# Performance work log

Measured on AMD Instinct MI355X. Metric: run time of the kernel, lower is better.

## Reference

```python
import jax, jax.numpy as jnp
import numpy as np

B, C, F = 4, 3, 5
HO, WO = 256, 256
HI, WI = HO + F - 1, WO + F - 1


def setup_inputs() -> dict:
    key = jax.random.key(0)
    k = jax.random.split(key, 6)
    return {
        "tensorInput": jax.random.normal(k[0], (B, C, HI, WI), dtype=jnp.float32),
        "tensorVertical": jax.random.uniform(k[1], (B, F, HO, WO), dtype=jnp.float32),
        "tensorHorizontal": jax.random.uniform(k[2], (B, F, HO, WO), dtype=jnp.float32),
        "tensorOffsetX": jax.random.normal(k[3], (B, F * F, HO, WO), dtype=jnp.float32),
        "tensorOffsetY": jax.random.normal(k[4], (B, F * F, HO, WO), dtype=jnp.float32),
        "tensorMask": jax.random.uniform(k[5], (B, F * F, HO, WO), dtype=jnp.float32),
    }


def _dsepconv(inp, vertical, horizontal, offset_x, offset_y, mask):
    b, c, hin, win = inp.shape
    f = vertical.shape[1]
    ho, wo = vertical.shape[2], vertical.shape[3]
    half = (f - 1) / 2.0

    fy = jnp.arange(f, dtype=inp.dtype).reshape(f, 1, 1, 1)
    fx = jnp.arange(f, dtype=inp.dtype).reshape(1, f, 1, 1)
    hg = jnp.arange(ho, dtype=inp.dtype).reshape(1, 1, ho, 1)
    wg = jnp.arange(wo, dtype=inp.dtype).reshape(1, 1, 1, wo)

    off_y = offset_y.reshape(b, f, f, ho, wo)  # note: code uses offset_y for delta_x
    off_x = offset_x.reshape(b, f, f, ho, wo)  # and offset_x for delta_y

    # sample positions per tap, [B,F,F,Ho,Wo]
    px = jnp.clip(off_y + wg + fx - half + 1.0, 0.0, win - 1)
    py = jnp.clip(off_x + hg + fy - half + 1.0, 0.0, hin - 1)

    left_f = jnp.floor(px)
    top_f = jnp.floor(py)
    wx = 1.0 - (px - left_f)  # bilinear weights
    wy = 1.0 - (py - top_f)

    l = left_f.astype(jnp.int32)
    t = top_f.astype(jnp.int32)
    r = jnp.minimum(l + 1, win - 1)
    btm = jnp.minimum(t + 1, hin - 1)

    def gather(img, yi, xi):
        return img[:, yi, xi]

    g = jax.vmap(gather)
    v_tl = g(inp, t, l)
    v_tr = g(inp, t, r)
    v_bl = g(inp, btm, l)
    v_br = g(inp, btm, r)

    wx_ = wx[:, None]  # add channel axis -> [B,1,F,F,Ho,Wo]
    wy_ = wy[:, None]
    val = (v_tl * wx_ * wy_ + v_tr * (1 - wx_) * wy_
           + v_bl * wx_ * (1 - wy_) + v_br * (1 - wx_) * (1 - wy_))

    # separable filter x mask per tap: [B,F,F,Ho,Wo]
    w_tap = vertical[:, :, None] * horizontal[:, None, :] * mask.reshape(b, f, f, ho, wo)
    # accumulate over the F*F taps
    return jnp.sum(val * w_tap[:, None], axis=(2, 3))  # [B,C,Ho,Wo]


def reference(tensorInput, tensorVertical, tensorHorizontal, tensorOffsetX, tensorOffsetY, tensorMask):
    return _dsepconv(tensorInput, tensorVertical, tensorHorizontal,
                     tensorOffsetX, tensorOffsetY, tensorMask)
```

## Files before the change

### kernel.cpp

```cpp
#include <hip/hip_runtime.h>
#include <hip/hip_fp16.h>

constexpr int B  = 4;
constexpr int C  = 3;
constexpr int F  = 5;
constexpr int HO = 256;
constexpr int WO = 256;
constexpr int HI = HO + F - 1;
constexpr int WI = WO + F - 1;
constexpr int P  = HO * WO;
constexpr int FF = F * F;
constexpr int PI = HI * WI;

constexpr int TROWS = 21;
constexpr int TCOLS = 80;
constexpr int TSTRIDE = 81;
constexpr int TN = TROWS * TCOLS;
constexpr int AMAX = (TROWS - 2) * TSTRIDE + (TCOLS - 2);

__device__ __forceinline__ uint2 pack3(float a, float b, float c) {
    __half2 ab = __floats2half2_rn(a, b);
    __half2 cz = __floats2half2_rn(c, 0.0f);
    uint2 r;
    r.x = *reinterpret_cast<const unsigned int*>(&ab);
    r.y = *reinterpret_cast<const unsigned int*>(&cz);
    return r;
}

__device__ __forceinline__ void fmacc(uint2 v, float w,
                                      float& a0, float& a1, float& a2) {
    __half2 ab = *reinterpret_cast<const __half2*>(&v.x);
    __half2 cz = *reinterpret_cast<const __half2*>(&v.y);
    a0 += __half2float(__low2half(ab))  * w;
    a1 += __half2float(__high2half(ab)) * w;
    a2 += __half2float(__low2half(cz))  * w;
}

__global__ __launch_bounds__(512, 8) void dsepconv_kernel(
    const float* __restrict__ inp,
    const float* __restrict__ vert,
    const float* __restrict__ horz,
    const float* __restrict__ offX,
    const float* __restrict__ offY,
    const float* __restrict__ mask,
    float* __restrict__ out)
{
    __shared__ uint2 tileq[TROWS * TSTRIDE];
    __shared__ float red[4][3][64];

    const int tid  = threadIdx.x;
    const int lane = tid & 63;
    const int wave = tid >> 6;
    const int wrow = wave >> 1;
    const int half = wave & 1;

    const int bx   = blockIdx.x;
    const int x0   = (bx & 3) * 64;
    const int y0   = ((bx >> 2) & 63) * 4;
    const int b    = bx >> 8;

    const float* in0 = inp + (size_t)b * C * PI;
    const float* in1 = in0 + PI;
    const float* in2 = in1 + PI;

    const int ry0 = y0 - 7;
    const int cx0 = x0 - 7;
#pragma unroll 1
    for (int e = tid; e < TN; e += 512) {
        int trow = e / TCOLS;
        int tcol = e - trow * TCOLS;
        int gy = min(max(ry0 + trow, 0), HI - 1);
        int gx = min(max(cx0 + tcol, 0), WI - 1);
        int g = gy * WI + gx;
        tileq[trow * TSTRIDE + tcol] = pack3(in0[g], in1[g], in2[g]);
    }
    __syncthreads();

    const int x   = x0 + lane;
    const int y   = y0 + wrow;
    const int pix = y * WO + x;

    const float* offXb = offX + (size_t)b * FF * P + pix;
    const float* offYb = offY + (size_t)b * FF * P + pix;
    const float* maskb = mask + (size_t)b * FF * P + pix;
    const float* vb    = vert + (size_t)b * F * P + pix;
    const float* hb    = horz + (size_t)b * F * P + pix;

    float acc0 = 0.f, acc1 = 0.f, acc2 = 0.f;

    const int k0 = half ? 12 : 0;
    const int k1 = half ? 25 : 12;

#pragma unroll 1
    for (int k = k0; k < k1; ++k) {
        const int i = k / F;
        const int j = k - i * F;

        float oy = offYb[k * P];
        float ox = offXb[k * P];
        float m  = maskb[k * P];
        float h  = hb[j * P];
        float v  = vb[i * P];

        float px = fminf(fmaxf(oy + (float)(x + j - 1), 0.0f), (float)(WI - 1));
        float py = fminf(fmaxf(ox + (float)(y + i - 1), 0.0f), (float)(HI - 1));

        float lf = floorf(px);
        float tf = floorf(py);
        int l = (int)lf;
        int t = (int)tf;
        float wx = 1.0f - (px - lf);
        float wy = 1.0f - (py - tf);

        float w   = v * h * m;
        float wyw = wy * w;
        float wbw = w - wyw;
        float wtl = wx * wyw;
        float wtr = wyw - wtl;
        float wbl = wx * wbw;
        float wbr = wbw - wbl;

        int lt = t - ry0;
        int ll = l - cx0;
        bool ok = ((unsigned)lt <= TROWS - 2) & ((unsigned)ll <= TCOLS - 2);

        int a = min(max(lt * TSTRIDE + ll, 0), AMAX);

        uint2 g_tl = tileq[a];
        uint2 g_tr = tileq[a + 1];
        uint2 g_bl = tileq[a + TSTRIDE];
        uint2 g_br = tileq[a + TSTRIDE + 1];

        if (__any(!ok)) {
            if (!ok) {
                int r  = min(l + 1, WI - 1);
                int bt = min(t + 1, HI - 1);
                int o_tl = t * WI + l,  o_tr = t * WI + r;
                int o_bl = bt * WI + l, o_br = bt * WI + r;
                g_tl = pack3(in0[o_tl], in1[o_tl], in2[o_tl]);
                g_tr = pack3(in0[o_tr], in1[o_tr], in2[o_tr]);
                g_bl = pack3(in0[o_bl], in1[o_bl], in2[o_bl]);
                g_br = pack3(in0[o_br], in1[o_br], in2[o_br]);
            }
        }

        fmacc(g_tl, wtl, acc0, acc1, acc2);
        fmacc(g_tr, wtr, acc0, acc1, acc2);
        fmacc(g_bl, wbl, acc0, acc1, acc2);
        fmacc(g_br, wbr, acc0, acc1, acc2);
    }

    if (half) {
        red[wrow][0][lane] = acc0;
        red[wrow][1][lane] = acc1;
        red[wrow][2][lane] = acc2;
    }
    __syncthreads();

    if (!half) {
        float* ob = out + (size_t)b * C * P + pix;
        ob[0]     = acc0 + red[wrow][0][lane];
        ob[P]     = acc1 + red[wrow][1][lane];
        ob[2 * P] = acc2 + red[wrow][2][lane];
    }
}

extern "C" void kernel_launch(void* const* d_in, const int* in_sizes, int n_in,
                              void* d_out, int out_size, void* d_ws, size_t ws_size,
                              hipStream_t stream) {
    const float* inp  = (const float*)d_in[0];
    const float* vert = (const float*)d_in[1];
    const float* horz = (const float*)d_in[2];
    const float* offX = (const float*)d_in[3];
    const float* offY = (const float*)d_in[4];
    const float* mask = (const float*)d_in[5];
    float* out = (float*)d_out;

    dim3 block(512);
    dim3 grid(B * (HO / 4) * (WO / 64));
    dsepconv_kernel<<<grid, block, 0, stream>>>(inp, vert, horz, offX, offY, mask, out);
}
```

Baseline: 26.54 us.

## Process two pixels per thread with float2 loads and prefetch next tap

Measured after the change: 24.75 us. 1.07x faster.

```diff
diff --git a/kernel.cpp b/kernel.cpp
--- a/kernel.cpp
+++ b/kernel.cpp
@@ -12,11 +12,15 @@
 constexpr int FF = F * F;
 constexpr int PI = HI * WI;
 
-constexpr int TROWS = 21;
-constexpr int TCOLS = 80;
-constexpr int TSTRIDE = 81;
+constexpr int TROWS = 19;
+constexpr int TCOLS = 145;
+constexpr int TSTRIDE = 149;
 constexpr int TN = TROWS * TCOLS;
 constexpr int AMAX = (TROWS - 2) * TSTRIDE + (TCOLS - 2);
+
+__device__ __forceinline__ float2 ld2(const float* p) {
+    return *reinterpret_cast<const float2*>(p);
+}
 
 __device__ __forceinline__ uint2 pack3(float a, float b, float c) {
     __half2 ab = __floats2half2_rn(a, b);
@@ -36,7 +40,7 @@
     a2 += __half2float(__low2half(cz))  * w;
 }
 
-__global__ __launch_bounds__(512, 8) void dsepconv_kernel(
+__global__ __launch_bounds__(256, 4) void dsepconv_kernel(
     const float* __restrict__ inp,
     const float* __restrict__ vert,
     const float* __restrict__ horz,
@@ -46,7 +50,7 @@
     float* __restrict__ out)
 {
     __shared__ uint2 tileq[TROWS * TSTRIDE];
-    __shared__ float red[4][3][64];
+    __shared__ float red[2][3][128];
 
     const int tid  = threadIdx.x;
     const int lane = tid & 63;
@@ -55,18 +59,41 @@
     const int half = wave & 1;
 
     const int bx   = blockIdx.x;
-    const int x0   = (bx & 3) * 64;
-    const int y0   = ((bx >> 2) & 63) * 4;
+    const int x0   = (bx & 1) * 128;
+    const int y0   = ((bx >> 1) & 127) * 2;
     const int b    = bx >> 8;
 
     const float* in0 = inp + (size_t)b * C * PI;
     const float* in1 = in0 + PI;
     const float* in2 = in1 + PI;
 
+    const int x   = x0 + 2 * lane;
+    const int y   = y0 + wrow;
+    const int pix = y * WO + x;
+
+    const float* offXb = offX + (size_t)b * FF * P + pix;
+    const float* offYb = offY + (size_t)b * FF * P + pix;
+    const float* maskb = mask + (size_t)b * FF * P + pix;
+    const float* vb    = vert + (size_t)b * F * P + pix;
+    const float* hb    = horz + (size_t)b * F * P + pix;
+
+    const int k0 = half ? 12 : 0;
+    const int k1 = half ? 25 : 12;
+
+    float2 oy, ox, m, h, v;
+    {
+        const int i = k0 / F, j = k0 - (k0 / F) * F;
+        oy = ld2(offYb + (size_t)k0 * P);
+        ox = ld2(offXb + (size_t)k0 * P);
+        m  = ld2(maskb + (size_t)k0 * P);
+        h  = ld2(hb + (size_t)j * P);
+        v  = ld2(vb + (size_t)i * P);
+    }
+
     const int ry0 = y0 - 7;
     const int cx0 = x0 - 7;
 #pragma unroll 1
-    for (int e = tid; e < TN; e += 512) {
+    for (int e = tid; e < TN; e += 256) {
         int trow = e / TCOLS;
         int tcol = e - trow * TCOLS;
         int gy = min(max(ry0 + trow, 0), HI - 1);
@@ -76,92 +103,118 @@
     }
     __syncthreads();
 
-    const int x   = x0 + lane;
-    const int y   = y0 + wrow;
-    const int pix = y * WO + x;
-
-    const float* offXb = offX + (size_t)b * FF * P + pix;
-    const float* offYb = offY + (size_t)b * FF * P + pix;
-    const float* maskb = mask + (size_t)b * FF * P + pix;
-    const float* vb    = vert + (size_t)b * F * P + pix;
-    const float* hb    = horz + (size_t)b * F * P + pix;
-
-    float acc0 = 0.f, acc1 = 0.f, acc2 = 0.f;
-
-    const int k0 = half ? 12 : 0;
-    const int k1 = half ? 25 : 12;
+    float acc0a = 0.f, acc1a = 0.f, acc2a = 0.f;
+    float acc0b = 0.f, acc1b = 0.f, acc2b = 0.f;
 
 #pragma unroll 1
     for (int k = k0; k < k1; ++k) {
         const int i = k / F;
         const int j = k - i * F;
 
-        float oy = offYb[k * P];
-        float ox = offXb[k * P];
-        float m  = maskb[k * P];
-        float h  = hb[j * P];
-        float v  = vb[i * P];
-
-        float px = fminf(fmaxf(oy + (float)(x + j - 1), 0.0f), (float)(WI - 1));
-        float py = fminf(fmaxf(ox + (float)(y + i - 1), 0.0f), (float)(HI - 1));
-
-        float lf = floorf(px);
-        float tf = floorf(py);
-        int l = (int)lf;
-        int t = (int)tf;
-        float wx = 1.0f - (px - lf);
-        float wy = 1.0f - (py - tf);
-
-        float w   = v * h * m;
-        float wyw = wy * w;
-        float wbw = w - wyw;
-        float wtl = wx * wyw;
-        float wtr = wyw - wtl;
-        float wbl = wx * wbw;
-        float wbr = wbw - wbl;
-
-        int lt = t - ry0;
-        int ll = l - cx0;
-        bool ok = ((unsigned)lt <= TROWS - 2) & ((unsigned)ll <= TCOLS - 2);
-
-        int a = min(max(lt * TSTRIDE + ll, 0), AMAX);
-
-        uint2 g_tl = tileq[a];
-        uint2 g_tr = tileq[a + 1];
-        uint2 g_bl = tileq[a + TSTRIDE];
-        uint2 g_br = tileq[a + TSTRIDE + 1];
-
-        if (__any(!ok)) {
-            if (!ok) {
-                int r  = min(l + 1, WI - 1);
-                int bt = min(t + 1, HI - 1);
-                int o_tl = t * WI + l,  o_tr = t * WI + r;
-                int o_bl = bt * WI + l, o_br = bt * WI + r;
-                g_tl = pack3(in0[o_tl], in1[o_tl], in2[o_tl]);
-                g_tr = pack3(in0[o_tr], in1[o_tr], in2[o_tr]);
-                g_bl = pack3(in0[o_bl], in1[o_bl], in2[o_bl]);
-                g_br = pack3(in0[o_br], in1[o_br], in2[o_br]);
+        const int kn  = (k + 1 < k1) ? k + 1 : k;
+        const int in_ = kn / F;
+        const int jn  = kn - in_ * F;
+        float2 oy_n = ld2(offYb + (size_t)kn * P);
+        float2 ox_n = ld2(offXb + (size_t)kn * P);
+        float2 m_n  = ld2(maskb + (size_t)kn * P);
+        float2 h_n  = ld2(hb + (size_t)jn * P);
+        float2 v_n  = ld2(vb + (size_t)in_ * P);
+
+        float pya = fminf(fmaxf(ox.x + (float)(y + i - 1), 0.0f), (float)(HI - 1));
+        float pyb = fminf(fmaxf(ox.y + (float)(y + i - 1), 0.0f), (float)(HI - 1));
+        float pxa = fminf(fmaxf(oy.x + (float)(x + j - 1), 0.0f), (float)(WI - 1));
+        float pxb = fminf(fmaxf(oy.y + (float)(x + j), 0.0f), (float)(WI - 1));
+
+        float lfa = floorf(pxa), tfa = floorf(pya);
+        float lfb = floorf(pxb), tfb = floorf(pyb);
+        int la = (int)lfa, ta = (int)tfa;
+        int lb = (int)lfb, tb = (int)tfb;
+        float wxa = 1.0f - (pxa - lfa), wya = 1.0f - (pya - tfa);
+        float wxb = 1.0f - (pxb - lfb), wyb = 1.0f - (pyb - tfb);
+
+        int lta = ta - ry0, lla = la - cx0;
+        int ltb = tb - ry0, llb = lb - cx0;
+        bool oka = ((unsigned)lta <= TROWS - 2) & ((unsigned)lla <= TCOLS - 2);
+        bool okb = ((unsigned)ltb <= TROWS - 2) & ((unsigned)llb <= TCOLS - 2);
+
+        int aa = min(max(lta * TSTRIDE + lla, 0), AMAX);
+        int ab = min(max(ltb * TSTRIDE + llb, 0), AMAX);
+
+        uint2 ga0 = tileq[aa];
+        uint2 ga1 = tileq[aa + 1];
+        uint2 ga2 = tileq[aa + TSTRIDE];
+        uint2 ga3 = tileq[aa + TSTRIDE + 1];
+        uint2 gb0 = tileq[ab];
+        uint2 gb1 = tileq[ab + 1];
+        uint2 gb2 = tileq[ab + TSTRIDE];
+        uint2 gb3 = tileq[ab + TSTRIDE + 1];
+
+        if (__any(!(oka & okb))) {
+            if (!oka) {
+                int r  = min(la + 1, WI - 1);
+                int bt = min(ta + 1, HI - 1);
+                int o0 = ta * WI + la, o1 = ta * WI + r;
+                int o2 = bt * WI + la, o3 = bt * WI + r;
+                ga0 = pack3(in0[o0], in1[o0], in2[o0]);
+                ga1 = pack3(in0[o1], in1[o1], in2[o1]);
+                ga2 = pack3(in0[o2], in1[o2], in2[o2]);
+                ga3 = pack3(in0[o3], in1[o3], in2[o3]);
+            }
+            if (!okb) {
+                int r  = min(lb + 1, WI - 1);
+                int bt = min(tb + 1, HI - 1);
+                int o0 = tb * WI + lb, o1 = tb * WI + r;
+                int o2 = bt * WI + lb, o3 = bt * WI + r;
+                gb0 = pack3(in0[o0], in1[o0], in2[o0]);
+                gb1 = pack3(in0[o1], in1[o1], in2[o1]);
+                gb2 = pack3(in0[o2], in1[o2], in2[o2]);
+                gb3 = pack3(in0[o3], in1[o3], in2[o3]);
             }
         }
 
-        fmacc(g_tl, wtl, acc0, acc1, acc2);
-        fmacc(g_tr, wtr, acc0, acc1, acc2);
-        fmacc(g_bl, wbl, acc0, acc1, acc2);
-        fmacc(g_br, wbr, acc0, acc1, acc2);
+        float wA   = v.x * h.x * m.x;
+        float wywA = wya * wA;
+        float wbwA = wA - wywA;
+        float wtlA = wxa * wywA;
+        float wtrA = wywA - wtlA;
+        float wblA = wxa * wbwA;
+        float wbrA = wbwA - wblA;
+
+        float wB   = v.y * h.y * m.y;
+        float wywB = wyb * wB;
+        float wbwB = wB - wywB;
+        float wtlB = wxb * wywB;
+        float wtrB = wywB - wtlB;
+        float wblB = wxb * wbwB;
+        float wbrB = wbwB - wblB;
+
+        fmacc(ga0, wtlA, acc0a, acc1a, acc2a);
+        fmacc(ga1, wtrA, acc0a, acc1a, acc2a);
+        fmacc(ga2, wblA, acc0a, acc1a, acc2a);
+        fmacc(ga3, wbrA, acc0a, acc1a, acc2a);
+        fmacc(gb0, wtlB, acc0b, acc1b, acc2b);
+        fmacc(gb1, wtrB, acc0b, acc1b, acc2b);
+        fmacc(gb2, wblB, acc0b, acc1b, acc2b);
+        fmacc(gb3, wbrB, acc0b, acc1b, acc2b);
+
+        oy = oy_n; ox = ox_n; m = m_n; h = h_n; v = v_n;
     }
 
     if (half) {
-        red[wrow][0][lane] = acc0;
-        red[wrow][1][lane] = acc1;
-        red[wrow][2][lane] = acc2;
+        *reinterpret_cast<float2*>(&red[wrow][0][2 * lane]) = make_float2(acc0a, acc0b);
+        *reinterpret_cast<float2*>(&red[wrow][1][2 * lane]) = make_float2(acc1a, acc1b);
+        *reinterpret_cast<float2*>(&red[wrow][2][2 * lane]) = make_float2(acc2a, acc2b);
     }
     __syncthreads();
 
     if (!half) {
         float* ob = out + (size_t)b * C * P + pix;
-        ob[0]     = acc0 + red[wrow][0][lane];
-        ob[P]     = acc1 + red[wrow][1][lane];
-        ob[2 * P] = acc2 + red[wrow][2][lane];
+        float2 r0 = *reinterpret_cast<const float2*>(&red[wrow][0][2 * lane]);
+        float2 r1 = *reinterpret_cast<const float2*>(&red[wrow][1][2 * lane]);
+        float2 r2 = *reinterpret_cast<const float2*>(&red[wrow][2][2 * lane]);
+        *reinterpret_cast<float2*>(&ob[0])     = make_float2(acc0a + r0.x, acc0b + r0.y);
+        *reinterpret_cast<float2*>(&ob[P])     = make_float2(acc1a + r1.x, acc1b + r1.y);
+        *reinterpret_cast<float2*>(&ob[2 * P]) = make_float2(acc2a + r2.x, acc2b + r2.y);
     }
 }
 
@@ -176,7 +229,7 @@
     const float* mask = (const float*)d_in[5];
     float* out = (float*)d_out;
 
-    dim3 block(512);
-    dim3 grid(B * (HO / 4) * (WO / 64));
+    dim3 block(256);
+    dim3 grid(B * (HO / 2) * (WO / 128));
     dsepconv_kernel<<<grid, block, 0, stream>>>(inp, vert, horz, offX, offY, mask, out);
 }
```
